# Optimization experiments

Hardware: AMD Instinct MI355X
Metric: run time of the kernel (lower is better)

Reference implementation:

```python
import jax, jax.numpy as jnp
import numpy as np

B, S = 16, 128
NQ, NC = 5000, 100
DK, DC = 128, 128  # dim_k == dim_e, dim_correct
N_AT, N_IT = 3600 + 1, 43200 + 1


def setup_inputs() -> dict:
    key = jax.random.key(0)
    ks = jax.random.split(key, 20)

    def xavier(k, shape):
        fan_in, fan_out = shape[0], shape[-1]
        lim = (6.0 / (fan_in + fan_out)) ** 0.5
        return jax.random.uniform(k, shape, jnp.float32, -lim, lim)

    inp = {
        'question_seq': jax.random.randint(ks[0], (B, S), 0, NQ),
        'use_time_seq': jax.random.randint(ks[1], (B, S), 0, N_AT - 1),
        'interval_time_seq': jax.random.randint(ks[2], (B, S), 0, N_IT - 1),
        'correct_seq': jax.random.uniform(ks[3], (B, S), jnp.float32),
        # binary-ish q-matrix with small smoothing offset (as in LPKT preprocessing)
        'q_matrix': jax.random.bernoulli(ks[4], 0.2, (NQ + 1, NC)).astype(jnp.float32) + 0.03,
        'h0': xavier(ks[5], (NC, DK)),  # xavier-init initial memory, shared across batch
        'e_w': xavier(ks[6], (NQ + 1, DK)),
        'at_w': xavier(ks[7], (N_AT, DK)),
        'it_w': xavier(ks[8], (N_IT, DK)),
        'W1': xavier(ks[9], (DC + 2 * DK, DK)), 'b1': jnp.zeros((DK,), jnp.float32),
        'W2': xavier(ks[10], (4 * DK, DK)), 'b2': jnp.zeros((DK,), jnp.float32),
        'W3': xavier(ks[11], (4 * DK, DK)), 'b3': jnp.zeros((DK,), jnp.float32),
        'W4': xavier(ks[12], (3 * DK, DK)), 'b4': jnp.zeros((DK,), jnp.float32),
        'W5': xavier(ks[13], (2 * DK, DK)), 'b5': jnp.zeros((DK,), jnp.float32),
    }
    return inp


def reference(question_seq, use_time_seq, interval_time_seq, correct_seq,
              q_matrix, h0, e_w, at_w, it_w,
              W1, b1, W2, b2, W3, b3, W4, b4, W5, b5):
    Bt, St = question_seq.shape
    dk = h0.shape[1]
    dc = W1.shape[0] - e_w.shape[1] - at_w.shape[1]

    e_emb = e_w[question_seq]              # [B,S,dk]
    at_emb = at_w[use_time_seq]            # [B,S,dk]
    it_emb = it_w[interval_time_seq]       # [B,S,dk]
    corr = jnp.broadcast_to(correct_seq[:, :, None], (Bt, St, dc))
    all_learning = jnp.concatenate([e_emb, at_emb, corr], -1) @ W1 + b1  # [B,S,dk]

    qm = q_matrix[question_seq]            # [B,S,nc]
    h_init = jnp.broadcast_to(h0, (Bt,) + h0.shape)          # [B,nc,dk]
    h_tilde0 = jnp.einsum('bn,nk->bk', qm[:, 0], h0)          # first q_e.bmm(h_pre)
    learning0 = jnp.zeros((Bt, dk), all_learning.dtype)

    # time-major xs for scan over t = 0 .. S-2
    xs = (jnp.swapaxes(qm[:, :-1], 0, 1),
          jnp.swapaxes(qm[:, 1:], 0, 1),
          jnp.swapaxes(it_emb[:, :-1], 0, 1),
          jnp.swapaxes(all_learning[:, :-1], 0, 1),
          jnp.swapaxes(e_emb[:, 1:], 0, 1))

    def step(carry, x):
        h, h_tilde_pre, learning_pre = carry
        q_e, q_next, it_t, learning, e_next = x
        x4 = jnp.concatenate([learning_pre, it_t, learning, h_tilde_pre], -1)  # [B,4dk]
        learning_gain = jnp.tanh(x4 @ W2 + b2)
        gamma_l = jax.nn.sigmoid(x4 @ W3 + b3)
        LG = gamma_l * (learning_gain + 1.0) * 0.5                 # [B,dk]
        LG_tilde = q_e[:, :, None] * LG[:, None, :]                 # outer prod [B,nc,dk]
        gf_in = jnp.concatenate([h,
                                 jnp.broadcast_to(LG[:, None, :], h.shape),
                                 jnp.broadcast_to(it_t[:, None, :], h.shape)], -1)
        gamma_f = jax.nn.sigmoid(gf_in @ W4 + b4)                   # [B,nc,dk]
        h_new = LG_tilde + gamma_f * h
        h_tilde = jnp.einsum('bn,bnk->bk', q_next, h_new)
        y = jnp.mean(jax.nn.sigmoid(jnp.concatenate([e_next, h_tilde], -1) @ W5 + b5), axis=-1)
        return (h_new, h_tilde, learning), y

    _, ys = jax.lax.scan(step, (h_init, h_tilde0, learning0), xs)   # ys: [S-1, B]
    pred = jnp.concatenate([jnp.zeros((Bt, 1), ys.dtype), ys.T], axis=1)  # pred[:,0]=0
    return pred
```

## Files before the change

kernel.cpp:

```cpp
#include <hip/hip_runtime.h>

constexpr int B  = 16;
constexpr int S  = 128;
constexpr int NC = 100;
constexpr int DK = 128;
constexpr int T  = S - 1;

typedef __attribute__((ext_vector_type(8))) short bf16x8;
typedef __attribute__((ext_vector_type(8))) unsigned short u16x8;
typedef __attribute__((ext_vector_type(4))) float f32x4;

__device__ __forceinline__ float sigm(float x) {
  return __builtin_amdgcn_rcpf(1.0f + __expf(-x));
}
__device__ __forceinline__ float tanh_fast(float x) {
  return 2.0f * __builtin_amdgcn_rcpf(1.0f + __expf(-2.0f * x)) - 1.0f;
}
__device__ __forceinline__ unsigned short f2bf(float x) {
  unsigned u = __float_as_uint(x);
  u += 0x7fff + ((u >> 16) & 1);
  return (unsigned short)(u >> 16);
}
__device__ __forceinline__ unsigned pkhi(float a, float b) {
  return __builtin_amdgcn_perm(__float_as_uint(b), __float_as_uint(a), 0x07060302u);
}
__device__ __forceinline__ float bfhi(unsigned short v) {
  return __uint_as_float(((unsigned)v) << 16);
}
__device__ __forceinline__ int pk(int k) { return k + ((k >> 5) << 2); }

__global__ void k_all_learning(const int* __restrict__ qs, const int* __restrict__ ats,
                               const float* __restrict__ corr,
                               const float* __restrict__ e_w, const float* __restrict__ at_w,
                               const float* __restrict__ W1, const float* __restrict__ b1,
                               float* __restrict__ AL) {
  int b = blockIdx.x >> 4, c = blockIdx.x & 15;
  int s0 = c * 8;
  int j = threadIdx.x;
  __shared__ float ve[8][DK], va[8][DK];
  __shared__ float cr[8];
#pragma unroll
  for (int i = 0; i < 8; ++i) {
    int bs = b * S + s0 + i;
    ve[i][j] = e_w[qs[bs] * DK + j];
    va[i][j] = at_w[ats[bs] * DK + j];
    if (j == 0) cr[i] = corr[bs];
  }
  __syncthreads();
  float acc[8];
  float cs = 0.0f;
#pragma unroll 4
  for (int k = 0; k < DK; ++k) cs += W1[(2 * DK + k) * DK + j];
  float bj = b1[j];
#pragma unroll
  for (int i = 0; i < 8; ++i) acc[i] = bj + cr[i] * cs;
#pragma unroll 2
  for (int k = 0; k < DK; ++k) {
    float we = W1[k * DK + j];
    float wa = W1[(DK + k) * DK + j];
#pragma unroll
    for (int i = 0; i < 8; ++i) {
      acc[i] = fmaf(ve[i][k], we, acc[i]);
      acc[i] = fmaf(va[i][k], wa, acc[i]);
    }
  }
#pragma unroll
  for (int i = 0; i < 8; ++i) AL[(b * S + s0 + i) * DK + j] = acc[i];
}

__global__ void k_consts(const int* __restrict__ qs, const int* __restrict__ its,
                         const float* __restrict__ it_w, const float* __restrict__ e_w,
                         const float* __restrict__ AL,
                         const float* __restrict__ W2, const float* __restrict__ b2,
                         const float* __restrict__ W3, const float* __restrict__ b3,
                         const float* __restrict__ W4, const float* __restrict__ b4,
                         const float* __restrict__ W5, const float* __restrict__ b5,
                         float* __restrict__ K2, float* __restrict__ K3,
                         float* __restrict__ C4, float* __restrict__ C5) {
  int b = blockIdx.x >> 4, c = blockIdx.x & 15;
  int t0 = c * 8;
  int nt = (t0 + 8 <= T) ? 8 : (T - t0);
  int j = threadIdx.x;
  __shared__ float lp[8][DK], itv[8][DK], lc[8][DK], en[8][DK];
  for (int i = 0; i < nt; ++i) {
    int bs = b * S + t0 + i;
    lp[i][j]  = (t0 + i == 0) ? 0.0f : AL[(bs - 1) * DK + j];
    lc[i][j]  = AL[bs * DK + j];
    itv[i][j] = it_w[its[bs] * DK + j];
    en[i][j]  = e_w[qs[bs + 1] * DK + j];
  }
  __syncthreads();
  float a2[8], a3[8], a4[8], a5[8];
  float v2 = b2[j], v3 = b3[j], v4 = b4[j], v5 = b5[j];
#pragma unroll
  for (int i = 0; i < 8; ++i) { a2[i] = v2; a3[i] = v3; a4[i] = v4; a5[i] = v5; }
#pragma unroll 2
  for (int k = 0; k < DK; ++k) {
    float w2a = W2[k * DK + j], w2b = W2[(DK + k) * DK + j], w2c = W2[(2 * DK + k) * DK + j];
    float w3a = W3[k * DK + j], w3b = W3[(DK + k) * DK + j], w3c = W3[(2 * DK + k) * DK + j];
    float w4c = W4[(2 * DK + k) * DK + j];
    float w5a = W5[k * DK + j];
#pragma unroll
    for (int i = 0; i < 8; ++i) {
      float vlp = lp[i][k], vit = itv[i][k], vlc = lc[i][k], ven = en[i][k];
      a2[i] = fmaf(vlp, w2a, a2[i]); a2[i] = fmaf(vit, w2b, a2[i]); a2[i] = fmaf(vlc, w2c, a2[i]);
      a3[i] = fmaf(vlp, w3a, a3[i]); a3[i] = fmaf(vit, w3b, a3[i]); a3[i] = fmaf(vlc, w3c, a3[i]);
      a4[i] = fmaf(vit, w4c, a4[i]);
      a5[i] = fmaf(ven, w5a, a5[i]);
    }
  }
  for (int i = 0; i < nt; ++i) {
    int o = (b * T + t0 + i) * DK + j;
    K2[o] = a2[i]; K3[o] = a3[i]; C4[o] = a4[i]; C5[o] = a5[i];
  }
}

__global__ __launch_bounds__(512, 2)
void k_scan(const int* __restrict__ qs,
            const float* __restrict__ qmat,
            const float* __restrict__ h0,
            const float* __restrict__ K2, const float* __restrict__ K3,
            const float* __restrict__ C4, const float* __restrict__ C5,
            const float* __restrict__ W2, const float* __restrict__ W3,
            const float* __restrict__ W4, const float* __restrict__ W5,
            float* __restrict__ out) {
  const int b   = blockIdx.x;
  const int tid = threadIdx.x;
  const int w   = tid >> 6;
  const int l   = tid & 63;
  const int l15 = l & 15;
  const int g   = l >> 4;
  const int wj  = w & 3;
  const int wn  = w >> 2;
  const int gc  = 16 * w + l15;
  const int kb  = 32 * g;
  const int ac  = 32 * wj + (l & 31);
  const int akb = (l >> 5) * 64;

  __shared__ alignas(16) unsigned short hBH[14336];
  __shared__ alignas(16) unsigned short hBL[14336];
  __shared__ alignas(16) unsigned short W4T[DK * 136];
  __shared__ alignas(16) unsigned short W5T[DK * 136];
  __shared__ alignas(16) float sLG[144];
  __shared__ alignas(16) float sHT[2][144];
  __shared__ alignas(16) float sQ[2][DK];
  __shared__ float sY[8];

  const float* W2d = W2 + 3 * DK * DK;
  const float* W3d = W3 + 3 * DK * DK;
  const float* W4a = W4;
  const float* W4b = W4 + DK * DK;
  const float* W5b = W5 + DK * DK;

  float w2r[32], w3r[32];
#pragma unroll
  for (int kk = 0; kk < 32; ++kk) {
    w2r[kk] = W2d[(kb + kk) * DK + gc];
    w3r[kk] = W3d[(kb + kk) * DK + gc];
  }

  for (int i = tid; i < DK * DK; i += 512) {
    int k = i >> 7, j = i & 127;
    W4T[j * 136 + k] = f2bf(W4b[i]);
    W5T[j * 136 + k] = f2bf(W5b[i]);
  }

  bf16x8 afr[2][4];
#pragma unroll
  for (int jt = 0; jt < 2; ++jt) {
    int j = 32 * wj + 16 * jt + l15;
#pragma unroll
    for (int ks = 0; ks < 4; ++ks) {
      bf16x8 v;
#pragma unroll
      for (int e = 0; e < 8; ++e) v[e] = (short)f2bf(W4a[(ks * 32 + g * 8 + e) * DK + j]);
      afr[jt][ks] = v;
    }
  }

  if (tid < DK) sQ[0][tid] = (tid < NC) ? qmat[qs[b * S] * NC + tid] : 0.0f;
  if (tid == 0) out[b * S] = 0.0f;
  if (tid < 144) { sHT[0][tid] = 0.0f; sHT[1][tid] = 0.0f; }

  float hold[2][4][4];
#pragma unroll
  for (int jt = 0; jt < 2; ++jt) {
    int j4 = 32 * wj + 16 * jt + 4 * g;
    int ks = j4 >> 5, lg = (j4 >> 3) & 3;
#pragma unroll
    for (int nt = 0; nt < 4; ++nt) {
      int ntg = 4 * wn + nt;
      if (ntg == 7) {
#pragma unroll
        for (int r = 0; r < 4; ++r) hold[jt][nt][r] = 0.0f;
        continue;
      }
      int n = 16 * ntg + l15;
      float x0 = (n < NC) ? h0[n * DK + j4 + 0] : 0.0f;
      float x1 = (n < NC) ? h0[n * DK + j4 + 1] : 0.0f;
      float x2 = (n < NC) ? h0[n * DK + j4 + 2] : 0.0f;
      float x3 = (n < NC) ? h0[n * DK + j4 + 3] : 0.0f;
      hold[jt][nt][0] = x0; hold[jt][nt][1] = x1;
      hold[jt][nt][2] = x2; hold[jt][nt][3] = x3;
      uint2 vh, vl;
      vh.x = pkhi(x0, x1); vh.y = pkhi(x2, x3);
      float l0 = x0 - __uint_as_float(__float_as_uint(x0) & 0xffff0000u);
      float l1 = x1 - __uint_as_float(__float_as_uint(x1) & 0xffff0000u);
      float l2 = x2 - __uint_as_float(__float_as_uint(x2) & 0xffff0000u);
      float l3 = x3 - __uint_as_float(__float_as_uint(x3) & 0xffff0000u);
      vl.x = pkhi(l0, l1); vl.y = pkhi(l2, l3);
      int idx = ((ntg * 4 + ks) * 64 + (lg << 4) + l15) * 8 + ((j4 & 4) ? 4 : 0);
      *(uint2*)&hBH[idx] = vh;
      *(uint2*)&hBL[idx] = vl;
    }
  }
  __syncthreads();

  {
#pragma unroll
    for (int jt = 0; jt < 2; ++jt) {
      int j4 = 32 * wj + 16 * jt + 4 * g;
      float htp[4] = {0.f, 0.f, 0.f, 0.f};
#pragma unroll
      for (int nt = 0; nt < 4; ++nt) {
        int ntg = 4 * wn + nt;
        if (ntg == 7) continue;
        int n = 16 * ntg + l15;
        float qe = sQ[0][n];
#pragma unroll
        for (int r = 0; r < 4; ++r) htp[r] = fmaf(qe, hold[jt][nt][r], htp[r]);
      }
#pragma unroll
      for (int r = 0; r < 4; ++r) {
        float v = htp[r];
        v += __shfl_xor(v, 1, 64); v += __shfl_xor(v, 2, 64);
        v += __shfl_xor(v, 4, 64); v += __shfl_xor(v, 8, 64);
        if (l15 == 0) atomicAdd(&sHT[0][pk(j4 + r)], v);
      }
    }
  }
  __syncthreads();

  float k2v = K2[(b * T) * DK + gc], k3v = K3[(b * T) * DK + gc];
  float c4_pf = C4[(b * T) * DK + ac];
  float c5_pf = C5[(b * T) * DK + gc];
  float c5_use = 0.0f;
  float qnew = (tid < NC) ? qmat[qs[b * S + 1] * NC + tid] : 0.0f;

  for (int t = 0; t < T; ++t) {
    const int cur = t & 1, nxt = cur ^ 1;


    f32x4 acc[2][4];
#pragma unroll
    for (int jt = 0; jt < 2; ++jt)
#pragma unroll
      for (int nt = 0; nt < 4; ++nt) acc[jt][nt] = (f32x4){0.f, 0.f, 0.f, 0.f};
#pragma unroll
    for (int nt = 0; nt < 4; ++nt) {
      int ntg = 4 * wn + nt;
      if (ntg == 7) continue;
      bf16x8 bh[4], bl[4];
#pragma unroll
      for (int ks = 0; ks < 4; ++ks) {
        bh[ks] = *(const bf16x8*)&hBH[(ntg * 4 + ks) * 512 + l * 8];
        bl[ks] = *(const bf16x8*)&hBL[(ntg * 4 + ks) * 512 + l * 8];
      }
#pragma unroll
      for (int ks = 0; ks < 4; ++ks)
#pragma unroll
        for (int jt = 0; jt < 2; ++jt) {
          acc[jt][nt] = __builtin_amdgcn_mfma_f32_16x16x32_bf16(afr[jt][ks], bh[ks], acc[jt][nt], 0, 0, 0);
          acc[jt][nt] = __builtin_amdgcn_mfma_f32_16x16x32_bf16(afr[jt][ks], bl[ks], acc[jt][nt], 0, 0, 0);
        }
    }

    if (t > 0) {
      float pa = 0.f, pb = 0.f;
#pragma unroll
      for (int mm = 0; mm < 4; ++mm) {
        u16x8 wv = *(const u16x8*)&W5T[gc * 136 + kb + 8 * mm];
        float4 h0v = *(const float4*)&sHT[cur][36 * g + 8 * mm];
        float4 h1v = *(const float4*)&sHT[cur][36 * g + 8 * mm + 4];
        pa = fmaf(h0v.x, bfhi(wv[0]), pa);
        pb = fmaf(h0v.y, bfhi(wv[1]), pb);
        pa = fmaf(h0v.z, bfhi(wv[2]), pa);
        pb = fmaf(h0v.w, bfhi(wv[3]), pb);
        pa = fmaf(h1v.x, bfhi(wv[4]), pa);
        pb = fmaf(h1v.y, bfhi(wv[5]), pb);
        pa = fmaf(h1v.z, bfhi(wv[6]), pa);
        pb = fmaf(h1v.w, bfhi(wv[7]), pb);
      }
      float p = pa + pb;
      p += __shfl_xor(p, 16, 64); p += __shfl_xor(p, 32, 64);
      float u = sigm(c5_use + p);
      u += __shfl_xor(u, 1, 64); u += __shfl_xor(u, 2, 64);
      u += __shfl_xor(u, 4, 64); u += __shfl_xor(u, 8, 64);
      if (l == 0) sY[w] = u;
    }

    {
      float p2a = 0.f, p2b = 0.f, p3a = 0.f, p3b = 0.f;
#pragma unroll
      for (int m = 0; m < 8; ++m) {
        float4 hv = *(const float4*)&sHT[cur][36 * g + 4 * m];
        p2a = fmaf(hv.x, w2r[4 * m + 0], p2a); p3a = fmaf(hv.x, w3r[4 * m + 0], p3a);
        p2b = fmaf(hv.y, w2r[4 * m + 1], p2b); p3b = fmaf(hv.y, w3r[4 * m + 1], p3b);
        p2a = fmaf(hv.z, w2r[4 * m + 2], p2a); p3a = fmaf(hv.z, w3r[4 * m + 2], p3a);
        p2b = fmaf(hv.w, w2r[4 * m + 3], p2b); p3b = fmaf(hv.w, w3r[4 * m + 3], p3b);
      }
      float p2 = p2a + p2b, p3 = p3a + p3b;
      p2 += __shfl_xor(p2, 16, 64); p2 += __shfl_xor(p2, 32, 64);
      p3 += __shfl_xor(p3, 16, 64); p3 += __shfl_xor(p3, 32, 64);
      if (l < 16) {
        float x2 = k2v + p2, x3 = k3v + p3;
        sLG[pk(gc)] = sigm(x3) * (tanh_fast(x2) + 1.0f) * 0.5f;
      }
      if (tid < DK) {
        sQ[nxt][tid] = qnew;
        sHT[nxt][pk(tid)] = 0.0f;
      }
    }
    __syncthreads();


    if (t > 0 && tid == 0) {
      float s = sY[0] + sY[1] + sY[2] + sY[3] + sY[4] + sY[5] + sY[6] + sY[7];
      out[b * S + t] = s * (1.0f / DK);
    }

    float c4_use = c4_pf;
    c5_use = c5_pf;
    {
      int tn  = (t + 1 < T) ? (t + 1) : (T - 1);
      int btn = (b * T + tn) * DK;
      k2v = K2[btn + gc]; k3v = K3[btn + gc];
      c4_pf = C4[btn + ac]; c5_pf = C5[btn + gc];
      int rq = (t + 2 < S) ? (t + 2) : (S - 1);
      qnew = (tid < NC) ? qmat[qs[b * S + rq] * NC + tid] : 0.0f;
    }

    float vv[2][4];
    {
      float pa = 0.f, pb = 0.f;
#pragma unroll
      for (int mm = 0; mm < 8; ++mm) {
        u16x8 wv = *(const u16x8*)&W4T[ac * 136 + akb + 8 * mm];
        float4 a0 = *(const float4*)&sLG[pk(akb + 8 * mm)];
        float4 a1 = *(const float4*)&sLG[pk(akb + 8 * mm + 4)];
        pa = fmaf(a0.x, bfhi(wv[0]), pa);
        pb = fmaf(a0.y, bfhi(wv[1]), pb);
        pa = fmaf(a0.z, bfhi(wv[2]), pa);
        pb = fmaf(a0.w, bfhi(wv[3]), pb);
        pa = fmaf(a1.x, bfhi(wv[4]), pa);
        pb = fmaf(a1.y, bfhi(wv[5]), pb);
        pa = fmaf(a1.z, bfhi(wv[6]), pa);
        pb = fmaf(a1.w, bfhi(wv[7]), pb);
      }
      float V = pa + pb;
      V += __shfl_xor(V, 32, 64);
      V += c4_use;
#pragma unroll
      for (int jt = 0; jt < 2; ++jt)
#pragma unroll
        for (int r = 0; r < 4; ++r)
          vv[jt][r] = __shfl(V, 16 * jt + 4 * g + r, 64);
    }

    {
#pragma unroll
      for (int jt = 0; jt < 2; ++jt) {
        int j4 = 32 * wj + 16 * jt + 4 * g;
        float4 a = *(const float4*)&sLG[pk(j4)];
        float lgv[4] = {a.x, a.y, a.z, a.w};
        float htpr[4] = {0.f, 0.f, 0.f, 0.f};
        int ks = j4 >> 5, lg = (j4 >> 3) & 3;
#pragma unroll
        for (int nt = 0; nt < 4; ++nt) {
          int ntg = 4 * wn + nt;
          if (ntg == 7) continue;
          int n = 16 * ntg + l15;
          float qe = sQ[cur][n], qn = sQ[nxt][n];
          float hn[4];
#pragma unroll
          for (int r = 0; r < 4; ++r) {
            float gf = sigm(acc[jt][nt][r] + vv[jt][r]);
            hn[r] = fmaf(gf, hold[jt][nt][r], qe * lgv[r]);
            hold[jt][nt][r] = hn[r];
            htpr[r] = fmaf(qn, hn[r], htpr[r]);
          }
          uint2 vh, vl;
          vh.x = pkhi(hn[0], hn[1]); vh.y = pkhi(hn[2], hn[3]);
          float l0 = hn[0] - __uint_as_float(__float_as_uint(hn[0]) & 0xffff0000u);
          float l1 = hn[1] - __uint_as_float(__float_as_uint(hn[1]) & 0xffff0000u);
          float l2 = hn[2] - __uint_as_float(__float_as_uint(hn[2]) & 0xffff0000u);
          float l3 = hn[3] - __uint_as_float(__float_as_uint(hn[3]) & 0xffff0000u);
          vl.x = pkhi(l0, l1); vl.y = pkhi(l2, l3);
          int idx = ((ntg * 4 + ks) * 64 + (lg << 4) + l15) * 8 + ((j4 & 4) ? 4 : 0);
          *(uint2*)&hBH[idx] = vh;
          *(uint2*)&hBL[idx] = vl;
        }
#pragma unroll
        for (int r = 0; r < 4; ++r) {
          float v = htpr[r];
          v += __shfl_xor(v, 1, 64); v += __shfl_xor(v, 2, 64);
          v += __shfl_xor(v, 4, 64); v += __shfl_xor(v, 8, 64);
          if (l15 == 0) atomicAdd(&sHT[nxt][pk(j4 + r)], v);
        }
      }
    }
    __syncthreads();
  }

  {
    const int fin = T & 1;
    float pa = 0.f, pb = 0.f;
#pragma unroll
    for (int mm = 0; mm < 4; ++mm) {
      u16x8 wv = *(const u16x8*)&W5T[gc * 136 + kb + 8 * mm];
      float4 h0v = *(const float4*)&sHT[fin][36 * g + 8 * mm];
      float4 h1v = *(const float4*)&sHT[fin][36 * g + 8 * mm + 4];
      pa = fmaf(h0v.x, bfhi(wv[0]), pa);
      pb = fmaf(h0v.y, bfhi(wv[1]), pb);
      pa = fmaf(h0v.z, bfhi(wv[2]), pa);
      pb = fmaf(h0v.w, bfhi(wv[3]), pb);
      pa = fmaf(h1v.x, bfhi(wv[4]), pa);
      pb = fmaf(h1v.y, bfhi(wv[5]), pb);
      pa = fmaf(h1v.z, bfhi(wv[6]), pa);
      pb = fmaf(h1v.w, bfhi(wv[7]), pb);
    }
    float p = pa + pb;
    p += __shfl_xor(p, 16, 64); p += __shfl_xor(p, 32, 64);
    float u = sigm(c5_use + p);
    u += __shfl_xor(u, 1, 64); u += __shfl_xor(u, 2, 64);
    u += __shfl_xor(u, 4, 64); u += __shfl_xor(u, 8, 64);
    if (l == 0) sY[w] = u;
  }
  __syncthreads();
  if (tid == 0) {
    float s = sY[0] + sY[1] + sY[2] + sY[3] + sY[4] + sY[5] + sY[6] + sY[7];
    out[b * S + T] = s * (1.0f / DK);
  }
}

extern "C" void kernel_launch(void* const* d_in, const int* in_sizes, int n_in,
                              void* d_out, int out_size, void* d_ws, size_t ws_size,
                              hipStream_t stream) {
  const int*   qs   = (const int*)d_in[0];
  const int*   ats  = (const int*)d_in[1];
  const int*   its  = (const int*)d_in[2];
  const float* corr = (const float*)d_in[3];
  const float* qmat = (const float*)d_in[4];
  const float* h0   = (const float*)d_in[5];
  const float* e_w  = (const float*)d_in[6];
  const float* at_w = (const float*)d_in[7];
  const float* it_w = (const float*)d_in[8];
  const float* W1 = (const float*)d_in[9];  const float* b1 = (const float*)d_in[10];
  const float* W2 = (const float*)d_in[11]; const float* b2 = (const float*)d_in[12];
  const float* W3 = (const float*)d_in[13]; const float* b3 = (const float*)d_in[14];
  const float* W4 = (const float*)d_in[15]; const float* b4 = (const float*)d_in[16];
  const float* W5 = (const float*)d_in[17]; const float* b5 = (const float*)d_in[18];
  float* out = (float*)d_out;

  float* AL = (float*)d_ws;
  float* K2 = AL + B * S * DK;
  float* K3 = K2 + B * T * DK;
  float* C4 = K3 + B * T * DK;
  float* C5 = C4 + B * T * DK;

  k_all_learning<<<dim3(B * 16), dim3(DK), 0, stream>>>(qs, ats, corr, e_w, at_w, W1, b1, AL);
  k_consts<<<dim3(B * 16), dim3(DK), 0, stream>>>(qs, its, it_w, e_w, AL,
                                                  W2, b2, W3, b3, W4, b4, W5, b5,
                                                  K2, K3, C4, C5);
  k_scan<<<dim3(B), dim3(512), 0, stream>>>(qs, qmat, h0, K2, K3, C4, C5,
                                            W2, W3, W4, W5, out);
}
```

Baseline: 689.6 us.

## Drop bf16 hi/lo split of h, keep W5 in registers, relayout W4 in LDS

The recurrent state h is now stored as a single bf16 copy with round-to-nearest (add 0x8000) instead of a high/low bf16 split. This halves the MFMA count and the LDS traffic for the gamma_f matmul. The W5 slice moves from an LDS bf16 table into per-thread fp32 registers, and W4 is laid out in LDS in k-chunk-major order. Together these cut per-step LDS reads, shared memory use and matrix work, but they reduce the accuracy of the recurrent matmul and raise register pressure.

```diff
diff --git a/kernel.cpp b/kernel.cpp
--- a/kernel.cpp
+++ b/kernel.cpp
@@ -21,8 +21,10 @@
   u += 0x7fff + ((u >> 16) & 1);
   return (unsigned short)(u >> 16);
 }
-__device__ __forceinline__ unsigned pkhi(float a, float b) {
-  return __builtin_amdgcn_perm(__float_as_uint(b), __float_as_uint(a), 0x07060302u);
+__device__ __forceinline__ unsigned pkrta(float a, float b) {
+  unsigned ua = __float_as_uint(a) + 0x8000u;
+  unsigned ub = __float_as_uint(b) + 0x8000u;
+  return __builtin_amdgcn_perm(ub, ua, 0x07060302u);
 }
 __device__ __forceinline__ float bfhi(unsigned short v) {
   return __uint_as_float(((unsigned)v) << 16);
@@ -138,9 +140,7 @@
   const int akb = (l >> 5) * 64;
 
   __shared__ alignas(16) unsigned short hBH[14336];
-  __shared__ alignas(16) unsigned short hBL[14336];
-  __shared__ alignas(16) unsigned short W4T[DK * 136];
-  __shared__ alignas(16) unsigned short W5T[DK * 136];
+  __shared__ alignas(16) unsigned short W4X[16 * 132 * 8];
   __shared__ alignas(16) float sLG[144];
   __shared__ alignas(16) float sHT[2][144];
   __shared__ alignas(16) float sQ[2][DK];
@@ -152,17 +152,17 @@
   const float* W4b = W4 + DK * DK;
   const float* W5b = W5 + DK * DK;
 
-  float w2r[32], w3r[32];
+  float w2r[32], w3r[32], w5r[32];
 #pragma unroll
   for (int kk = 0; kk < 32; ++kk) {
     w2r[kk] = W2d[(kb + kk) * DK + gc];
     w3r[kk] = W3d[(kb + kk) * DK + gc];
+    w5r[kk] = W5b[(kb + kk) * DK + gc];
   }
 
   for (int i = tid; i < DK * DK; i += 512) {
     int k = i >> 7, j = i & 127;
-    W4T[j * 136 + k] = f2bf(W4b[i]);
-    W5T[j * 136 + k] = f2bf(W5b[i]);
+    W4X[((k >> 3) * 132 + j) * 8 + (k & 7)] = f2bf(W4b[i]);
   }
 
   bf16x8 afr[2][4];
@@ -202,16 +202,10 @@
       float x3 = (n < NC) ? h0[n * DK + j4 + 3] : 0.0f;
       hold[jt][nt][0] = x0; hold[jt][nt][1] = x1;
       hold[jt][nt][2] = x2; hold[jt][nt][3] = x3;
-      uint2 vh, vl;
-      vh.x = pkhi(x0, x1); vh.y = pkhi(x2, x3);
-      float l0 = x0 - __uint_as_float(__float_as_uint(x0) & 0xffff0000u);
-      float l1 = x1 - __uint_as_float(__float_as_uint(x1) & 0xffff0000u);
-      float l2 = x2 - __uint_as_float(__float_as_uint(x2) & 0xffff0000u);
-      float l3 = x3 - __uint_as_float(__float_as_uint(x3) & 0xffff0000u);
-      vl.x = pkhi(l0, l1); vl.y = pkhi(l2, l3);
+      uint2 vh;
+      vh.x = pkrta(x0, x1); vh.y = pkrta(x2, x3);
       int idx = ((ntg * 4 + ks) * 64 + (lg << 4) + l15) * 8 + ((j4 & 4) ? 4 : 0);
       *(uint2*)&hBH[idx] = vh;
-      *(uint2*)&hBL[idx] = vl;
     }
   }
   __syncthreads();
@@ -260,36 +254,26 @@
     for (int nt = 0; nt < 4; ++nt) {
       int ntg = 4 * wn + nt;
       if (ntg == 7) continue;
-      bf16x8 bh[4], bl[4];
-#pragma unroll
-      for (int ks = 0; ks < 4; ++ks) {
+      bf16x8 bh[4];
+#pragma unroll
+      for (int ks = 0; ks < 4; ++ks)
         bh[ks] = *(const bf16x8*)&hBH[(ntg * 4 + ks) * 512 + l * 8];
-        bl[ks] = *(const bf16x8*)&hBL[(ntg * 4 + ks) * 512 + l * 8];
-      }
 #pragma unroll
       for (int ks = 0; ks < 4; ++ks)
 #pragma unroll
-        for (int jt = 0; jt < 2; ++jt) {
+        for (int jt = 0; jt < 2; ++jt)
           acc[jt][nt] = __builtin_amdgcn_mfma_f32_16x16x32_bf16(afr[jt][ks], bh[ks], acc[jt][nt], 0, 0, 0);
-          acc[jt][nt] = __builtin_amdgcn_mfma_f32_16x16x32_bf16(afr[jt][ks], bl[ks], acc[jt][nt], 0, 0, 0);
-        }
     }
 
     if (t > 0) {
       float pa = 0.f, pb = 0.f;
 #pragma unroll
-      for (int mm = 0; mm < 4; ++mm) {
-        u16x8 wv = *(const u16x8*)&W5T[gc * 136 + kb + 8 * mm];
-        float4 h0v = *(const float4*)&sHT[cur][36 * g + 8 * mm];
-        float4 h1v = *(const float4*)&sHT[cur][36 * g + 8 * mm + 4];
-        pa = fmaf(h0v.x, bfhi(wv[0]), pa);
-        pb = fmaf(h0v.y, bfhi(wv[1]), pb);
-        pa = fmaf(h0v.z, bfhi(wv[2]), pa);
-        pb = fmaf(h0v.w, bfhi(wv[3]), pb);
-        pa = fmaf(h1v.x, bfhi(wv[4]), pa);
-        pb = fmaf(h1v.y, bfhi(wv[5]), pb);
-        pa = fmaf(h1v.z, bfhi(wv[6]), pa);
-        pb = fmaf(h1v.w, bfhi(wv[7]), pb);
+      for (int m = 0; m < 8; ++m) {
+        float4 hv = *(const float4*)&sHT[cur][36 * g + 4 * m];
+        pa = fmaf(hv.x, w5r[4 * m + 0], pa);
+        pb = fmaf(hv.y, w5r[4 * m + 1], pb);
+        pa = fmaf(hv.z, w5r[4 * m + 2], pa);
+        pb = fmaf(hv.w, w5r[4 * m + 3], pb);
       }
       float p = pa + pb;
       p += __shfl_xor(p, 16, 64); p += __shfl_xor(p, 32, 64);
@@ -345,7 +329,8 @@
       float pa = 0.f, pb = 0.f;
 #pragma unroll
       for (int mm = 0; mm < 8; ++mm) {
-        u16x8 wv = *(const u16x8*)&W4T[ac * 136 + akb + 8 * mm];
+        int kc = (akb >> 3) + mm;
+        u16x8 wv = *(const u16x8*)&W4X[(kc * 132 + ac) * 8];
         float4 a0 = *(const float4*)&sLG[pk(akb + 8 * mm)];
         float4 a1 = *(const float4*)&sLG[pk(akb + 8 * mm + 4)];
         pa = fmaf(a0.x, bfhi(wv[0]), pa);
@@ -389,16 +374,10 @@
             hold[jt][nt][r] = hn[r];
             htpr[r] = fmaf(qn, hn[r], htpr[r]);
           }
-          uint2 vh, vl;
-          vh.x = pkhi(hn[0], hn[1]); vh.y = pkhi(hn[2], hn[3]);
-          float l0 = hn[0] - __uint_as_float(__float_as_uint(hn[0]) & 0xffff0000u);
-          float l1 = hn[1] - __uint_as_float(__float_as_uint(hn[1]) & 0xffff0000u);
-          float l2 = hn[2] - __uint_as_float(__float_as_uint(hn[2]) & 0xffff0000u);
-          float l3 = hn[3] - __uint_as_float(__float_as_uint(hn[3]) & 0xffff0000u);
-          vl.x = pkhi(l0, l1); vl.y = pkhi(l2, l3);
+          uint2 vh;
+          vh.x = pkrta(hn[0], hn[1]); vh.y = pkrta(hn[2], hn[3]);
           int idx = ((ntg * 4 + ks) * 64 + (lg << 4) + l15) * 8 + ((j4 & 4) ? 4 : 0);
           *(uint2*)&hBH[idx] = vh;
-          *(uint2*)&hBL[idx] = vl;
         }
 #pragma unroll
         for (int r = 0; r < 4; ++r) {
@@ -416,18 +395,12 @@
     const int fin = T & 1;
     float pa = 0.f, pb = 0.f;
 #pragma unroll
-    for (int mm = 0; mm < 4; ++mm) {
-      u16x8 wv = *(const u16x8*)&W5T[gc * 136 + kb + 8 * mm];
-      float4 h0v = *(const float4*)&sHT[fin][36 * g + 8 * mm];
-      float4 h1v = *(const float4*)&sHT[fin][36 * g + 8 * mm + 4];
-      pa = fmaf(h0v.x, bfhi(wv[0]), pa);
-      pb = fmaf(h0v.y, bfhi(wv[1]), pb);
-      pa = fmaf(h0v.z, bfhi(wv[2]), pa);
-      pb = fmaf(h0v.w, bfhi(wv[3]), pb);
-      pa = fmaf(h1v.x, bfhi(wv[4]), pa);
-      pb = fmaf(h1v.y, bfhi(wv[5]), pb);
-      pa = fmaf(h1v.z, bfhi(wv[6]), pa);
-      pb = fmaf(h1v.w, bfhi(wv[7]), pb);
+    for (int m = 0; m < 8; ++m) {
+      float4 hv = *(const float4*)&sHT[fin][36 * g + 4 * m];
+      pa = fmaf(hv.x, w5r[4 * m + 0], pa);
+      pb = fmaf(hv.y, w5r[4 * m + 1], pb);
+      pa = fmaf(hv.z, w5r[4 * m + 2], pa);
+      pb = fmaf(hv.w, w5r[4 * m + 3], pb);
     }
     float p = pa + pb;
     p += __shfl_xor(p, 16, 64); p += __shfl_xor(p, 32, 64);
```

After: 794.0 us. +15.1%, slower.
